# Performance work log

Hardware: AMD Instinct MI355X
Metric: run time of the kernel (lower is better)

Reference implementation:

```python
import jax, jax.numpy as jnp
import numpy as np

B, C, H, W = 8, 256, 64, 64
HID = 4 * C          # mlp_ratio = 4
M = C // 8           # KAttention scale = 8
EPS = 1e-6


def setup_inputs() -> dict:
    key = jax.random.key(0)
    ks = jax.random.split(key, 24)
    n = lambda k, s, sc=1.0: jax.random.normal(k, s, dtype=jnp.float32) * sc
    return {
        "x": n(ks[0], (B, C, H, W)),
        "y": n(ks[1], (B, C, H, W)),
        # shared SeparableConvBN(dim, dim, k=3): 1x1 conv -> depthwise 3x3 -> BN(eval, folded to scale/shift)
        "conv_pw_w": n(ks[2], (C, C), 0.05),
        "conv_dw_w": n(ks[3], (C, 1, 3, 3), 0.1),
        "conv_bn_s": 1.0 + n(ks[4], (C,), 0.1),
        "conv_bn_t": n(ks[5], (C,), 0.1),
        # shared BatchNorm2d(dim) `self.norm` (eval mode, folded)
        "norm_s": 1.0 + n(ks[6], (C,), 0.1),
        "norm_t": n(ks[7], (C,), 0.1),
        # KAttention 1x1 convs (no bias) + gamma
        "q_w": n(ks[8], (M, C), 0.05),
        "k_w": n(ks[9], (M, C), 0.05),
        "v_w": n(ks[10], (C, C), 0.05),
        "gamma_k": n(ks[11], (1,), 0.1),
        # CAttention gamma
        "gamma_c": n(ks[12], (1,), 0.1),
        # Mlp: ConvBN(1x1, bias) -> ReLU6 -> ConvBN(1x1, bias); dropout = identity (eval)
        "fc1_w": n(ks[13], (HID, C), 0.05),
        "fc1_b": n(ks[14], (HID,), 0.05),
        "bn1_s": 1.0 + n(ks[15], (HID,), 0.1),
        "bn1_t": n(ks[16], (HID,), 0.1),
        "fc2_w": n(ks[17], (C, HID), 0.05),
        "fc2_b": n(ks[18], (C,), 0.05),
        "bn2_s": 1.0 + n(ks[19], (C,), 0.1),
        "bn2_t": n(ks[20], (C,), 0.1),
    }


def _bn(x, s, t):
    return x * s[None, :, None, None] + t[None, :, None, None]


def _c1(x, w, b=None):
    # 1x1 conv as channel matmul: [B,C,H,W] x [O,C] -> [B,O,H,W]
    out = jnp.einsum('bchw,oc->bohw', x, w)
    return out if b is None else out + b[None, :, None, None]


def _dw3(x, w):
    # depthwise 3x3, padding=1
    return jax.lax.conv_general_dilated(
        x, w, window_strides=(1, 1), padding='SAME',
        feature_group_count=x.shape[1],
        dimension_numbers=('NCHW', 'OIHW', 'NCHW'))


def reference(x, y, conv_pw_w, conv_dw_w, conv_bn_s, conv_bn_t, norm_s, norm_t,
              q_w, k_w, v_w, gamma_k, gamma_c,
              fc1_w, fc1_b, bn1_s, bn1_t, fc2_w, fc2_b, bn2_s, bn2_t):

    def sepconvbn(z):
        return _bn(_dw3(_c1(z, conv_pw_w), conv_dw_w), conv_bn_s, conv_bn_t)

    def norm(z):
        return _bn(z, norm_s, norm_t)

    def katt(z):
        b, c, h, w = z.shape
        N = h * w
        Q = jax.nn.softplus(_c1(z, q_w)).reshape(b, M, N).transpose(0, 2, 1)  # [b,N,m]
        K = jax.nn.softplus(_c1(z, k_w)).reshape(b, M, N)                    # [b,m,N]
        V = _c1(z, v_w).reshape(b, c, N)                                     # [b,c,N]
        KV = jnp.einsum('bmn,bcn->bmc', K, V)                                # [b,m,c]
        inv = 1.0 / jnp.einsum('bnm,bm->bn', Q, K.sum(-1) + EPS)            # [b,N]
        wv = jnp.einsum('bnm,bmc,bn->bcn', Q, KV, inv)                       # [b,c,N]
        return z + gamma_k[0] * wv.reshape(b, c, h, w)

    def catt(z):
        b, c, h, w = z.shape
        f = z.reshape(b, c, h * w)
        energy = jnp.einsum('bcn,bdn->bcd', f, f)                            # [b,c,c]
        att = jax.nn.softmax(energy.max(-1, keepdims=True) - energy, axis=-1)
        out = jnp.einsum('bcd,bdn->bcn', att, f).reshape(b, c, h, w)
        return gamma_c[0] * out + z

    def light(z):
        return katt(z) + catt(z)

    def mlp(z):
        hdn = jnp.clip(_bn(_c1(z, fc1_w, fc1_b), bn1_s, bn1_t), 0.0, 6.0)  # ReLU6
        return _bn(_c1(hdn, fc2_w, fc2_b), bn2_s, bn2_t)

    x1 = norm(sepconvbn(x))
    ax1 = light(x1)
    y1 = norm(sepconvbn(y))
    ay1 = light(y1)
    x2 = mlp(norm(x1 * ay1))
    y2 = mlp(norm(y1 * ax1))
    y3 = y + y2
    x3 = x + x2 + y3
    return (x3, y3)
```

## Files before the change

### kernel.cpp

```cpp
#include <hip/hip_runtime.h>
#include <hip/hip_bf16.h>
#include <math.h>

typedef __hip_bfloat16 bf16;
typedef unsigned short u16;
#define DEV __device__ __forceinline__

DEV float tofl(float v){ return v; }
DEV float tofl(bf16 v){ return __bfloat162float(v); }
DEV bf16  f2b(float v){ return __float2bfloat16(v); }
DEV u16   f2bu(float v){ bf16 h = f2b(v); u16 u; __builtin_memcpy(&u,&h,2); return u; }
DEV float u2f(u16 u){ bf16 h; __builtin_memcpy(&h,&u,2); return __bfloat162float(h); }

static constexpr int Cc=256, Nn=4096, Mm=32;
static constexpr size_t ACT = (size_t)8*Cc*Nn;
static constexpr float EPSc = 1e-6f;

typedef __attribute__((ext_vector_type(8))) __bf16 bf16x8;
typedef __attribute__((ext_vector_type(4))) float  f32x4;

struct StageRegs { int4 a[4], b[4]; };

DEV void stage_load(const u16* __restrict__ gA, int ldA,
                    const u16* __restrict__ gB, int ldB, int tid, StageRegs& r)
{
  int row = tid>>3, g = tid&7;
#pragma unroll
  for(int i=0;i<4;i++){
    r.a[i] = *(const int4*)(gA + (size_t)(row+32*i)*ldA + g*8);
    r.b[i] = *(const int4*)(gB + (size_t)(row+32*i)*ldB + g*8);
  }
}
DEV void stage_write(u16* __restrict__ sA, u16* __restrict__ sB,
                     int tid, const StageRegs& r)
{
  int row = tid>>3, g = tid&7;
#pragma unroll
  for(int i=0;i<4;i++){
    int rr = row+32*i;
    int gg = ((g ^ (rr&7))<<3);
    *(int4*)(sA + rr*64 + gg) = r.a[i];
    *(int4*)(sB + rr*64 + gg) = r.b[i];
  }
}

template<int KDIM, int OMODE>
__global__ __launch_bounds__(256,2) void gemm_bf16(
    const u16* __restrict__ A, long sAb,
    const u16* __restrict__ B,
    float* __restrict__ Cf, u16* __restrict__ Cb,
    const float* __restrict__ bia, const float* __restrict__ scl,
    const float* __restrict__ sht)
{
  __shared__ __align__(16) u16 sA[2][8192];
  __shared__ __align__(16) u16 sB[2][8192];
  int tid = threadIdx.x;
  int nt = blockIdx.x, mt = blockIdx.y, b = blockIdx.z;
  const u16* gA = A + (size_t)b*sAb + (size_t)mt*128*KDIM;
  const u16* gB = B + ((size_t)b*4096 + (size_t)nt*128)*KDIM;
  int w = tid>>6, l = tid&63;
  int wr = w>>1, wc = w&1;
  int l15 = l&15, lg = l>>4;
  f32x4 acc[4][4] = {};
  StageRegs r;
  stage_load(gA, KDIM, gB, KDIM, tid, r);
  stage_write(sA[0], sB[0], tid, r);
  __syncthreads();
  constexpr int NT = KDIM/64;
  for(int t=0;t<NT;t++){
    int cur = t&1;
    if(t+1<NT) stage_load(gA + (t+1)*64, KDIM, gB + (t+1)*64, KDIM, tid, r);
#pragma unroll
    for(int ks=0;ks<2;ks++){
      bf16x8 af[4], bfr[4];
#pragma unroll
      for(int m=0;m<4;m++){
        int row = wr*64 + m*16 + l15;
        int g = ks*4 + lg;
        af[m] = *(const bf16x8*)(&sA[cur][row*64 + ((g^(row&7))<<3)]);
      }
#pragma unroll
      for(int nn=0;nn<4;nn++){
        int row = wc*64 + nn*16 + l15;
        int g = ks*4 + lg;
        bfr[nn] = *(const bf16x8*)(&sB[cur][row*64 + ((g^(row&7))<<3)]);
      }
#pragma unroll
      for(int m=0;m<4;m++)
#pragma unroll
        for(int nn=0;nn<4;nn++)
          acc[m][nn] = __builtin_amdgcn_mfma_f32_16x16x32_bf16(af[m], bfr[nn], acc[m][nn], 0,0,0);
    }
    if(t+1<NT) stage_write(sA[cur^1], sB[cur^1], tid, r);
    __syncthreads();
  }
  int obase = mt*128 + wr*64;
  int nbase = nt*128 + wc*64;
  if (OMODE==0){
    size_t Mrows = (size_t)gridDim.y*128;
#pragma unroll
    for(int m=0;m<4;m++)
#pragma unroll
      for(int nn=0;nn<4;nn++){
        int o_ = obase + m*16 + (lg<<2);
        int n_ = nbase + nn*16 + l15;
        float* dst = Cf + (((size_t)b*Mrows + o_)<<12) + n_;
#pragma unroll
        for(int i=0;i<4;i++) dst[(size_t)i<<12] = acc[m][nn][i];
      }
  } else {
#pragma unroll
    for(int m=0;m<4;m++)
#pragma unroll
      for(int nn=0;nn<4;nn++){
        int o_ = obase + m*16 + (lg<<2);
        int n_ = nbase + nn*16 + l15;
        union { u16 u[4]; uint2 v; } pk;
#pragma unroll
        for(int i=0;i<4;i++){
          int o = o_+i;
          float a2 = (acc[m][nn][i] + bia[o])*scl[o] + sht[o];
          pk.u[i] = f2bu(fminf(fmaxf(a2,0.f),6.f));
        }
        *(uint2*)(Cb + ((size_t)b*4096 + (size_t)n_)*1024 + o_) = pk.v;
      }
  }
}

template<int KTILES, int KSPLIT, int OMODE>
__global__ __launch_bounds__(256,2) void gemm3(
    const u16* __restrict__ Ah, const u16* __restrict__ Al, int ldA, long sAb,
    const u16* __restrict__ Bh, const u16* __restrict__ Bl, int ldB, long sBb,
    float* __restrict__ Cf)
{
  __shared__ __align__(16) u16 sA[2][8192];
  __shared__ __align__(16) u16 sB[2][8192];
  int tid = threadIdx.x;
  int nt = blockIdx.x, mt = blockIdx.y;
  int b  = blockIdx.z / KSPLIT, ks = blockIdx.z % KSPLIT;
  long koff = (long)ks * (KTILES*64);
  const u16* A0 = Ah + (size_t)b*sAb + (size_t)mt*128*ldA + koff;
  const u16* A1 = Al + (size_t)b*sAb + (size_t)mt*128*ldA + koff;
  const u16* B0 = Bh + (size_t)b*sBb + (size_t)nt*128*ldB + koff;
  const u16* B1 = Bl + (size_t)b*sBb + (size_t)nt*128*ldB + koff;
  int w = tid>>6, l = tid&63;
  int wr = w>>1, wc = w&1;
  int l15 = l&15, lg = l>>4;
  f32x4 acc[4][4] = {};
  StageRegs r;
  for(int pass=0; pass<3; ++pass){
    const u16* gA = (pass==2) ? A1 : A0;
    const u16* gB = (pass==1) ? B1 : B0;
    stage_load(gA, ldA, gB, ldB, tid, r);
    stage_write(sA[0], sB[0], tid, r);
    __syncthreads();
    for(int t=0;t<KTILES;t++){
      int cur = t&1;
      if(t+1<KTILES) stage_load(gA + (t+1)*64, ldA, gB + (t+1)*64, ldB, tid, r);
#pragma unroll
      for(int kss=0;kss<2;kss++){
        bf16x8 af[4], bfr[4];
#pragma unroll
        for(int m=0;m<4;m++){
          int row = wr*64 + m*16 + l15;
          int g = kss*4 + lg;
          af[m] = *(const bf16x8*)(&sA[cur][row*64 + ((g^(row&7))<<3)]);
        }
#pragma unroll
        for(int nn=0;nn<4;nn++){
          int row = wc*64 + nn*16 + l15;
          int g = kss*4 + lg;
          bfr[nn] = *(const bf16x8*)(&sB[cur][row*64 + ((g^(row&7))<<3)]);
        }
#pragma unroll
        for(int m=0;m<4;m++)
#pragma unroll
          for(int nn=0;nn<4;nn++)
            acc[m][nn] = __builtin_amdgcn_mfma_f32_16x16x32_bf16(af[m], bfr[nn], acc[m][nn], 0,0,0);
      }
      if(t+1<KTILES) stage_write(sA[cur^1], sB[cur^1], tid, r);
      __syncthreads();
    }
  }
  int obase = mt*128 + wr*64;
  int nbase = nt*128 + wc*64;
  if (OMODE==0){
    size_t Mrows = (size_t)gridDim.y*128;
#pragma unroll
    for(int m=0;m<4;m++)
#pragma unroll
      for(int nn=0;nn<4;nn++){
        int o_ = obase + m*16 + (lg<<2);
        int n_ = nbase + nn*16 + l15;
        float* dst = Cf + (((size_t)b*Mrows + o_)<<12) + n_;
#pragma unroll
        for(int i=0;i<4;i++) dst[(size_t)i<<12] = acc[m][nn][i];
      }
  } else {
    int gridB = gridDim.z / KSPLIT;
    float* Cb = Cf + ((size_t)ks*gridB + b)*65536;
#pragma unroll
    for(int m=0;m<4;m++)
#pragma unroll
      for(int nn=0;nn<4;nn++){
        int o_ = obase + m*16 + (lg<<2);
        int n_ = nbase + nn*16 + l15;
#pragma unroll
        for(int i=0;i<4;i++) Cb[(size_t)(o_+i)*256 + n_] = acc[m][nn][i];
      }
  }
}

__global__ __launch_bounds__(256) void cvt_w(const float* __restrict__ s,
    u16* __restrict__ d)
{
  int i = blockIdx.x*256 + threadIdx.x;
  d[i] = f2bu(s[i]);
}
__global__ __launch_bounds__(256) void cvt_wsplit(const float* __restrict__ s,
    u16* __restrict__ dh, u16* __restrict__ dl)
{
  int i = blockIdx.x*256 + threadIdx.x;
  float v = s[i];
  u16 h = f2bu(v);
  dh[i] = h; dl[i] = f2bu(v - u2f(h));
}
__global__ __launch_bounds__(256) void cvt_split_nm(const float* __restrict__ x,
    u16* __restrict__ xh, u16* __restrict__ xl)
{
  int n  = blockIdx.x*256 + threadIdx.x;
  int c0 = blockIdx.y*16;
  int b  = blockIdx.z;
  union { u16 u[16]; uint4 q[2]; } ph, pl;
#pragma unroll
  for (int oo=0;oo<16;oo++){
    float v = x[(((size_t)b*256 + c0 + oo)<<12) + n];
    u16 h = f2bu(v);
    ph.u[oo] = h; pl.u[oo] = f2bu(v - u2f(h));
  }
  size_t o = (((size_t)b*4096 + n)<<8) + c0;
  *(uint4*)(xh+o) = ph.q[0]; *(uint4*)(xh+o+8) = ph.q[1];
  *(uint4*)(xl+o) = pl.q[0]; *(uint4*)(xl+o+8) = pl.q[1];
}
__global__ __launch_bounds__(256) void cvt_transpose(const u16* __restrict__ zc,
    u16* __restrict__ zn)
{
  int n  = blockIdx.x*256 + threadIdx.x;
  int c0 = blockIdx.y*16;
  int b  = blockIdx.z;
  union { u16 u[16]; uint4 q[2]; } pk;
#pragma unroll
  for (int oo=0;oo<16;oo++)
    pk.u[oo] = zc[(((size_t)b*256 + c0 + oo)<<12) + n];
  u16* dst = zn + (((size_t)b*4096 + n)<<8) + c0;
  *(uint4*)dst       = pk.q[0];
  *(uint4*)(dst + 8) = pk.q[1];
}

__global__ __launch_bounds__(256) void dw_norm_split(const float* __restrict__ pw,
    u16* __restrict__ zh, u16* __restrict__ zl, const float* __restrict__ dww,
    const float* __restrict__ cbs, const float* __restrict__ cbt,
    const float* __restrict__ ns, const float* __restrict__ nt)
{
  size_t idx = (size_t)blockIdx.x*256 + threadIdx.x;
  int n = (int)(idx & 4095);
  int c = (int)((idx>>12) & 255);
  int h = n>>6, wq = n&63;
  const float* p = pw + (idx - n);
  float acc = 0.f;
  for(int i=0;i<3;i++){
    int hh = h+i-1; if((unsigned)hh >= 64u) continue;
    for(int j=0;j<3;j++){
      int ww = wq+j-1; if((unsigned)ww >= 64u) continue;
      acc += dww[c*9 + i*3 + j] * p[hh*64 + ww];
    }
  }
  float bn = acc*cbs[c] + cbt[c];
  float v  = bn*ns[c] + nt[c];
  u16 hi = f2bu(v);
  zh[idx] = hi; zl[idx] = f2bu(v - u2f(hi));
}

DEV void mac16hl(const u16* __restrict__ hb, const u16* __restrict__ lb,
                 const float* __restrict__ wb, float* __restrict__ acc)
{
  for (int k=0;k<256;k+=4){
    float a0 = u2f(hb[(size_t)(k+0)<<12]) + u2f(lb[(size_t)(k+0)<<12]);
    float a1 = u2f(hb[(size_t)(k+1)<<12]) + u2f(lb[(size_t)(k+1)<<12]);
    float a2 = u2f(hb[(size_t)(k+2)<<12]) + u2f(lb[(size_t)(k+2)<<12]);
    float a3 = u2f(hb[(size_t)(k+3)<<12]) + u2f(lb[(size_t)(k+3)<<12]);
#pragma unroll
    for (int oo=0;oo<16;oo++){
      const float* wr = wb + (size_t)oo*256 + k;
      acc[oo] = fmaf(a3,wr[3],fmaf(a2,wr[2],fmaf(a1,wr[1],fmaf(a0,wr[0],acc[oo]))));
    }
  }
}

__global__ __launch_bounds__(256) void qk_tile(const u16* __restrict__ zh,
    const u16* __restrict__ zl, const float* __restrict__ qw,
    const float* __restrict__ kw, float* __restrict__ Qf, float* __restrict__ Kf)
{
  int n  = blockIdx.x*256 + threadIdx.x;
  int y  = blockIdx.y;
  int o0 = (y&1)*16;
  int b  = blockIdx.z;
  const float* w   = (y<2) ? qw : kw;
  float*       out = (y<2) ? Qf : Kf;
  const u16* hb = zh + (((size_t)b*256)<<12) + n;
  const u16* lb = zl + (((size_t)b*256)<<12) + n;
  float acc[16] = {};
  mac16hl(hb, lb, w + (size_t)o0*256, acc);
#pragma unroll
  for (int oo=0;oo<16;oo++){
    float a = acc[oo];
    a = fmaxf(a,0.f) + log1pf(expf(-fabsf(a)));
    out[(((size_t)b*32 + o0 + oo)<<12) + n] = a;
  }
}

DEV int swz(int r, int j){ return r*128 + ((j ^ ((r>>2)&7))<<2); }

__global__ __launch_bounds__(256) void syrk32(const float* __restrict__ Kf,
    const float* __restrict__ V, float* __restrict__ Cp)
{
  int dt = blockIdx.x, ks = blockIdx.y, b = blockIdx.z;
  __shared__ __align__(16) float sa[32*128];
  __shared__ __align__(16) float sb[32*128];
  int tx = threadIdx.x & 15, ty = threadIdx.x >> 4;
  const float* Ab = Kf + (((size_t)b*32)<<12);
  const float* Bb = V  + (((size_t)b*256 + dt*32)<<12);
  float acc[2][2] = {};
  for (int k0 = ks<<10; k0 < (ks<<10)+1024; k0 += 128){
    __syncthreads();
#pragma unroll
    for (int i=0;i<4;i++){
      int fi = threadIdx.x + i*256;
      int r = fi >> 5, j = fi & 31;
      *(float4*)&sa[swz(r,j)] = *(const float4*)&Ab[((size_t)r<<12) + k0 + (j<<2)];
      *(float4*)&sb[swz(r,j)] = *(const float4*)&Bb[((size_t)r<<12) + k0 + (j<<2)];
    }
    __syncthreads();
#pragma unroll 4
    for (int jj=0;jj<32;jj++){
      float4 av[2], bv[2];
#pragma unroll
      for (int i=0;i<2;i++) av[i] = *(const float4*)&sa[swz(2*ty+i,jj)];
#pragma unroll
      for (int i=0;i<2;i++) bv[i] = *(const float4*)&sb[swz(2*tx+i,jj)];
#pragma unroll
      for (int i=0;i<2;i++)
#pragma unroll
        for (int j2=0;j2<2;j2++)
          acc[i][j2] = fmaf(av[i].w,bv[j2].w, fmaf(av[i].z,bv[j2].z,
                       fmaf(av[i].y,bv[j2].y, fmaf(av[i].x,bv[j2].x, acc[i][j2]))));
    }
  }
  float* Cb = Cp + ((size_t)ks*8 + b)*8192;
#pragma unroll
  for (int i=0;i<2;i++)
#pragma unroll
    for (int j2=0;j2<2;j2++)
      Cb[(size_t)(2*ty+i)*256 + dt*32 + 2*tx + j2] = acc[i][j2];
}

__global__ __launch_bounds__(256) void kv_combine(const float* __restrict__ p,
    float* __restrict__ o)
{
  int i = blockIdx.x*256 + threadIdx.x;
  o[i] = p[i] + p[i+65536] + p[i+131072] + p[i+196608];
}

__global__ __launch_bounds__(256) void softmax16(const float* __restrict__ Ep,
    u16* __restrict__ att)
{
  int bc = blockIdx.x;
  int b = bc>>8, c = bc&255;
  size_t base = (size_t)b*65536 + (size_t)c*256;
  int d = threadIdx.x;
  float ed = 0.f;
#pragma unroll
  for(int ks=0;ks<16;ks++) ed += Ep[base + (size_t)ks*524288 + d];
  __shared__ float red[4];
  int lane = d&63, wid = d>>6;
  float v = ed;
  for (int off=32;off;off>>=1) v = fmaxf(v, __shfl_down(v,off));
  if(lane==0) red[wid]=v;
  __syncthreads();
  float rowmax = fmaxf(fmaxf(red[0],red[1]),fmaxf(red[2],red[3]));
  __syncthreads();
  float s = rowmax - ed;
  float v2 = s;
  for (int off=32;off;off>>=1) v2 = fmaxf(v2, __shfl_down(v2,off));
  if(lane==0) red[wid]=v2;
  __syncthreads();
  float smax = fmaxf(fmaxf(red[0],red[1]),fmaxf(red[2],red[3]));
  __syncthreads();
  float p = expf(s - smax);
  float sv = p;
  for (int off=32;off;off>>=1) sv += __shfl_down(sv,off);
  if(lane==0) red[wid]=sv;
  __syncthreads();
  float sum = red[0]+red[1]+red[2]+red[3];
  att[((size_t)bc<<8)+d] = f2bu(p/sum);
}

__global__ __launch_bounds__(256) void catt_px(const u16* __restrict__ zh,
    const u16* __restrict__ zl, const u16* __restrict__ oh,
    const u16* __restrict__ ol, const float* __restrict__ Qf,
    const float* __restrict__ KVf, const float* __restrict__ invb,
    const float* __restrict__ s1b, const float* __restrict__ gkp,
    const float* __restrict__ gcp, const float* __restrict__ ns,
    const float* __restrict__ nt, u16* __restrict__ px)
{
  int n  = blockIdx.x*256 + threadIdx.x;
  int c0 = blockIdx.y*16;
  int b  = blockIdx.z;
  const float* qb  = Qf  + (((size_t)b*Mm)<<12) + n;
  const float* kvb = KVf + ((size_t)b<<13) + c0;
  float s2[16] = {};
#pragma unroll
  for (int m=0;m<Mm;m++){
    float qm = qb[(size_t)m<<12];
#pragma unroll
    for (int oo=0;oo<16;oo++) s2[oo] = fmaf(qm, kvb[m*256 + oo], s2[oo]);
  }
  float invv = invb[((size_t)b<<12)+n];
  float gk = gkp[0], gc = gcp[0];
  union { u16 u[16]; uint4 q[2]; } pk;
#pragma unroll
  for (int oo=0;oo<16;oo++){
    int c = c0+oo;
    size_t idx = (((size_t)b*256 + c)<<12) + n;
    float zv = u2f(zh[idx]) + u2f(zl[idx]);
    float ov = u2f(oh[idx]) + u2f(ol[idx]);
    float a = 2.f*zv + gc*s1b[idx] + gk*s2[oo]*invv;
    pk.u[oo] = f2bu(ov*a*ns[c] + nt[c]);
  }
  u16* dst = px + (((size_t)b*4096 + n)<<8) + c0;
  *(uint4*)dst       = pk.q[0];
  *(uint4*)(dst + 8) = pk.q[1];
}

__global__ __launch_bounds__(256) void rowsum_lit(const float* __restrict__ A, float* __restrict__ out)
{
  int x = blockIdx.x;
  const float* ar = A + ((size_t)x << 12);
  float a = 0.f;
  for(int n=threadIdx.x; n<Nn; n+=256) a += ar[n];
  __shared__ float red[4];
  for(int off=32;off;off>>=1) a += __shfl_down(a,off);
  int lane = threadIdx.x&63, wid = threadIdx.x>>6;
  if(lane==0) red[wid]=a;
  __syncthreads();
  if(threadIdx.x==0) out[x] = red[0]+red[1]+red[2]+red[3];
}

__global__ __launch_bounds__(256) void inv_lit(const float* __restrict__ Qf,
    const float* __restrict__ Ks, float* __restrict__ invb)
{
  size_t idx = (size_t)blockIdx.x*256 + threadIdx.x;
  int b = (int)(idx>>12);
  const float* qb = Qf + ((size_t)b*Mm << 12) + (int)(idx&4095);
  const float* ks = Ks + b*Mm;
  float s = 0.f;
  for(int m=0;m<Mm;m++) s += qb[(size_t)m<<12]*(ks[m]+EPSc);
  invb[idx] = 1.f/s;
}

__global__ __launch_bounds__(256) void final_y(const float* __restrict__ yin,
    const float* __restrict__ acc, const float* __restrict__ b2,
    const float* __restrict__ s2, const float* __restrict__ t2, float* __restrict__ out)
{
  size_t idx = (size_t)blockIdx.x*256 + threadIdx.x;
  int c = (int)((idx>>12) & 255);
  float y2 = (acc[idx] + b2[c])*s2[c] + t2[c];
  out[ACT + idx] = yin[idx] + y2;
}

__global__ __launch_bounds__(256) void final_x(const float* __restrict__ xin,
    const float* __restrict__ acc, const float* __restrict__ b2,
    const float* __restrict__ s2, const float* __restrict__ t2, float* __restrict__ out)
{
  size_t idx = (size_t)blockIdx.x*256 + threadIdx.x;
  int c = (int)((idx>>12) & 255);
  float x2 = (acc[idx] + b2[c])*s2[c] + t2[c];
  out[idx] = xin[idx] + x2 + out[ACT + idx];
}

extern "C" void kernel_launch(void* const* d_in, const int* in_sizes, int n_in,
                              void* d_out, int out_size, void* d_ws, size_t ws_size,
                              hipStream_t stream)
{
  (void)in_sizes; (void)n_in; (void)out_size; (void)ws_size;
  const float* xin  = (const float*)d_in[0];
  const float* yin  = (const float*)d_in[1];
  const float* pw_w = (const float*)d_in[2];
  const float* dw_w = (const float*)d_in[3];
  const float* cbs  = (const float*)d_in[4];
  const float* cbt  = (const float*)d_in[5];
  const float* ns   = (const float*)d_in[6];
  const float* nt   = (const float*)d_in[7];
  const float* q_w  = (const float*)d_in[8];
  const float* k_w  = (const float*)d_in[9];
  const float* v_w  = (const float*)d_in[10];
  const float* gk   = (const float*)d_in[11];
  const float* gc   = (const float*)d_in[12];
  const float* fc1_w= (const float*)d_in[13];
  const float* fc1_b= (const float*)d_in[14];
  const float* bn1s = (const float*)d_in[15];
  const float* bn1t = (const float*)d_in[16];
  const float* fc2_w= (const float*)d_in[17];
  const float* fc2_b= (const float*)d_in[18];
  const float* bn2s = (const float*)d_in[19];
  const float* bn2t = (const float*)d_in[20];

  char* ws = (char*)d_ws;
  float* A     = (float*)(ws);
  u16*   x1h   = (u16*)  (ws + 33554432);
  u16*   x1l   = (u16*)  (ws + 50331648);
  u16*   y1h   = (u16*)  (ws + 67108864);
  u16*   y1l   = (u16*)  (ws + 83886080);
  u16*   hid   = (u16*)  (ws + 33554432);
  u16*   px_y  = (u16*)  (ws + 100663296);
  u16*   px_x  = (u16*)  (ws + 117440512);
  u16*   xh_nm = (u16*)  (ws + 100663296);
  u16*   xl_nm = (u16*)  (ws + 117440512);
  u16*   z1b   = (u16*)  (ws + 117440512);
  float* Qf    = (float*)(ws + 134217728);
  float* Kf    = (float*)(ws + 138412032);
  u16*   pwh   = (u16*)  (ws + 134217728);
  u16*   pwl   = (u16*)  (ws + 134217728 + 131072);
  u16*   attb  = (u16*)  (ws + 142606336);
  u16*   fc1wb = (u16*)  (ws + 142606336);
  u16*   fc2wb = (u16*)  (ws + 142606336 + 524288);
  float* KVf   = (float*)(ws + 143654912);
  float* Ksf   = (float*)(ws + 143917056);
  float* invb  = (float*)(ws + 143918080);
  float* KVp   = (float*)(ws + 144049152);
  u16*   vwb   = (u16*)  (ws + 144049152);
  float* Ep    = A;
  float* accb  = A;

  dim3 blk(256);
  dim3 gPX(16,16,8), gQK(16,4,8), gKV(8,4,8);
  dim3 gPW(32,2,8), gEn(2,2,128), gG256(32,2,8), gFC1(32,8,8), gFC2(32,2,8);

  cvt_wsplit<<<dim3(256),blk,0,stream>>>(pw_w, pwh, pwl);
  for (int im=0;im<2;im++){
    const float* in = (im==0) ? xin : yin;
    u16* zh = (im==0) ? x1h : y1h;
    u16* zl = (im==0) ? x1l : y1l;
    cvt_split_nm<<<gPX,blk,0,stream>>>(in, xh_nm, xl_nm);
    gemm3<4,1,0><<<gPW,blk,0,stream>>>(pwh, pwl, 256, 0,
                                       xh_nm, xl_nm, 256, 1048576, A);
    dw_norm_split<<<dim3(32768),blk,0,stream>>>(A, zh, zl, dw_w, cbs, cbt, ns, nt);
  }

  for (int t=0;t<2;t++){
    const u16* zh = (t==0) ? x1h : y1h;
    const u16* zl = (t==0) ? x1l : y1l;
    const u16* oh = (t==0) ? y1h : x1h;
    const u16* ol = (t==0) ? y1l : x1l;
    u16* pxout    = (t==0) ? px_y : px_x;
    cvt_w<<<dim3(256),blk,0,stream>>>(v_w, vwb);
    cvt_transpose<<<gPX,blk,0,stream>>>(zh, z1b);
    qk_tile<<<gQK,blk,0,stream>>>(zh, zl, q_w, k_w, Qf, Kf);
    gemm_bf16<256,0><<<gG256,blk,0,stream>>>(vwb, 0, z1b, A, nullptr,
                                             nullptr, nullptr, nullptr);
    syrk32<<<gKV,blk,0,stream>>>(Kf, A, KVp);
    kv_combine<<<dim3(256),blk,0,stream>>>(KVp, KVf);
    rowsum_lit<<<dim3(256),blk,0,stream>>>(Kf, Ksf);
    inv_lit<<<dim3(128),blk,0,stream>>>(Qf, Ksf, invb);
    gemm3<4,16,2><<<gEn,blk,0,stream>>>(zh, zl, 4096, 1048576,
                                        zh, zl, 4096, 1048576, Ep);
    softmax16<<<dim3(2048),blk,0,stream>>>(Ep, attb);
    gemm_bf16<256,0><<<gG256,blk,0,stream>>>(attb, 65536, z1b, A, nullptr,
                                             nullptr, nullptr, nullptr);
    catt_px<<<gPX,blk,0,stream>>>(zh, zl, oh, ol, Qf, KVf, invb, A,
                                  gk, gc, ns, nt, pxout);
  }

  cvt_w<<<dim3(1024),blk,0,stream>>>(fc1_w, fc1wb);
  cvt_w<<<dim3(1024),blk,0,stream>>>(fc2_w, fc2wb);
  for (int s=0;s<2;s++){
    const u16* px = (s==0) ? px_y : px_x;
    gemm_bf16<256,1><<<gFC1,blk,0,stream>>>(fc1wb, 0, px, nullptr, hid,
                                            fc1_b, bn1s, bn1t);
    gemm_bf16<1024,0><<<gFC2,blk,0,stream>>>(fc2wb, 0, hid, accb, nullptr,
                                             nullptr, nullptr, nullptr);
    if (s==0) final_y<<<dim3(32768),blk,0,stream>>>(yin, accb, fc2_b, bn2s, bn2t, (float*)d_out);
    else      final_x<<<dim3(32768),blk,0,stream>>>(xin, accb, fc2_b, bn2s, bn2t, (float*)d_out);
  }
}
```

Before: 865.7 us.

## Move Q/K projection and KV reduction onto bf16 MFMA GEMMs with bf16 intermediates

Replaces the scalar FMA qk_tile and fp32 syrk32 kernels with MFMA-based bf16 GEMMs. Q and K weights are packed into one padded 128-row operand, and K is also written in bf16 so the KV product runs on matrix cores with a 16-way k-split. V and the channel-attention output are now stored as bf16 instead of fp32, halving their write and read traffic. Weight conversion is hoisted out of the loop. The cost is lower precision for Q/K (single bf16 instead of hi/lo split), K, V and the attention output, and half the MFMA work in the padded Q/K and KV GEMMs is discarded.

```diff
diff --git a/kernel.cpp b/kernel.cpp
--- a/kernel.cpp
+++ b/kernel.cpp
@@ -7,7 +7,6 @@
 #define DEV __device__ __forceinline__
 
 DEV float tofl(float v){ return v; }
-DEV float tofl(bf16 v){ return __bfloat162float(v); }
 DEV bf16  f2b(float v){ return __float2bfloat16(v); }
 DEV u16   f2bu(float v){ bf16 h = f2b(v); u16 u; __builtin_memcpy(&u,&h,2); return u; }
 DEV float u2f(u16 u){ bf16 h; __builtin_memcpy(&h,&u,2); return __bfloat162float(h); }
@@ -108,7 +107,7 @@
 #pragma unroll
         for(int i=0;i<4;i++) dst[(size_t)i<<12] = acc[m][nn][i];
       }
-  } else {
+  } else if (OMODE==1){
 #pragma unroll
     for(int m=0;m<4;m++)
 #pragma unroll
@@ -124,7 +123,163 @@
         }
         *(uint2*)(Cb + ((size_t)b*4096 + (size_t)n_)*1024 + o_) = pk.v;
       }
-  }
+  } else {
+    size_t Mrows = (size_t)gridDim.y*128;
+#pragma unroll
+    for(int m=0;m<4;m++)
+#pragma unroll
+      for(int nn=0;nn<4;nn++){
+        int o_ = obase + m*16 + (lg<<2);
+        int n_ = nbase + nn*16 + l15;
+        u16* dst = Cb + (((size_t)b*Mrows + o_)<<12) + n_;
+#pragma unroll
+        for(int i=0;i<4;i++) dst[(size_t)i<<12] = f2bu(acc[m][nn][i]);
+      }
+  }
+}
+
+__global__ __launch_bounds__(256,2) void qk_gemm(
+    const u16* __restrict__ Aqk, const u16* __restrict__ B,
+    float* __restrict__ Qf, float* __restrict__ Kf, u16* __restrict__ Kb)
+{
+  __shared__ __align__(16) u16 sA[2][8192];
+  __shared__ __align__(16) u16 sB[2][8192];
+  int tid = threadIdx.x;
+  int nt = blockIdx.x, b = blockIdx.z;
+  const u16* gA = Aqk;
+  const u16* gB = B + ((size_t)b*4096 + (size_t)nt*128)*256;
+  int w = tid>>6, l = tid&63;
+  int wr = w>>1, wc = w&1;
+  int l15 = l&15, lg = l>>4;
+  f32x4 acc[4][4] = {};
+  StageRegs r;
+  stage_load(gA, 256, gB, 256, tid, r);
+  stage_write(sA[0], sB[0], tid, r);
+  __syncthreads();
+  for(int t=0;t<4;t++){
+    int cur = t&1;
+    if(t+1<4) stage_load(gA + (t+1)*64, 256, gB + (t+1)*64, 256, tid, r);
+#pragma unroll
+    for(int ks=0;ks<2;ks++){
+      bf16x8 af[4], bfr[4];
+#pragma unroll
+      for(int m=0;m<4;m++){
+        int row = wr*64 + m*16 + l15;
+        int g = ks*4 + lg;
+        af[m] = *(const bf16x8*)(&sA[cur][row*64 + ((g^(row&7))<<3)]);
+      }
+#pragma unroll
+      for(int nn=0;nn<4;nn++){
+        int row = wc*64 + nn*16 + l15;
+        int g = ks*4 + lg;
+        bfr[nn] = *(const bf16x8*)(&sB[cur][row*64 + ((g^(row&7))<<3)]);
+      }
+#pragma unroll
+      for(int m=0;m<4;m++)
+#pragma unroll
+        for(int nn=0;nn<4;nn++)
+          acc[m][nn] = __builtin_amdgcn_mfma_f32_16x16x32_bf16(af[m], bfr[nn], acc[m][nn], 0,0,0);
+    }
+    if(t+1<4) stage_write(sA[cur^1], sB[cur^1], tid, r);
+    __syncthreads();
+  }
+  if (wr!=0) return;
+  int nbase = nt*128 + wc*64;
+#pragma unroll
+  for(int m=0;m<4;m++)
+#pragma unroll
+    for(int nn=0;nn<4;nn++){
+      int o_ = m*16 + (lg<<2);
+      int n_ = nbase + nn*16 + l15;
+#pragma unroll
+      for(int i=0;i<4;i++){
+        float a = acc[m][nn][i];
+        a = fmaxf(a,0.f) + log1pf(expf(-fabsf(a)));
+        if (m<2){
+          Qf[(((size_t)b*32 + o_+i)<<12) + n_] = a;
+        } else {
+          int kr = o_+i-32;
+          Kf[(((size_t)b*32 + kr)<<12) + n_] = a;
+          Kb[(((size_t)b*32 + kr)<<12) + n_] = f2bu(a);
+        }
+      }
+    }
+}
+
+__global__ __launch_bounds__(256,2) void kv_gemm(const u16* __restrict__ Kb,
+    const u16* __restrict__ Vb, float* __restrict__ Cp)
+{
+  __shared__ __align__(16) u16 sA[2][8192];
+  __shared__ __align__(16) u16 sB[2][8192];
+  int tid = threadIdx.x;
+  int nt = blockIdx.x;
+  int b  = blockIdx.z >> 4, ks = blockIdx.z & 15;
+  const u16* gA = Kb + ((size_t)b*32)*4096 + ks*256;
+  const u16* gB = Vb + ((size_t)b*256 + (size_t)nt*128)*4096 + ks*256;
+  int row = tid>>3, g = tid&7;
+  int w = tid>>6, l = tid&63;
+  int wr = w>>1, wc = w&1;
+  int l15 = l&15, lg = l>>4;
+  f32x4 acc[4][4] = {};
+  StageRegs r;
+#define KV_LOAD(koff) do { \
+    _Pragma("unroll") \
+    for(int i=0;i<4;i++){ \
+      r.a[i] = *(const int4*)(gA + (size_t)row*4096 + (koff) + g*8); \
+      r.b[i] = *(const int4*)(gB + (size_t)(row+32*i)*4096 + (koff) + g*8); \
+    } } while(0)
+  KV_LOAD(0);
+  stage_write(sA[0], sB[0], tid, r);
+  __syncthreads();
+  for(int t=0;t<4;t++){
+    int cur = t&1;
+    if(t+1<4) KV_LOAD((t+1)*64);
+#pragma unroll
+    for(int kss=0;kss<2;kss++){
+      bf16x8 af[4], bfr[4];
+#pragma unroll
+      for(int m=0;m<4;m++){
+        int rr = wr*64 + m*16 + l15;
+        int gg = kss*4 + lg;
+        af[m] = *(const bf16x8*)(&sA[cur][rr*64 + ((gg^(rr&7))<<3)]);
+      }
+#pragma unroll
+      for(int nn=0;nn<4;nn++){
+        int rr = wc*64 + nn*16 + l15;
+        int gg = kss*4 + lg;
+        bfr[nn] = *(const bf16x8*)(&sB[cur][rr*64 + ((gg^(rr&7))<<3)]);
+      }
+#pragma unroll
+      for(int m=0;m<4;m++)
+#pragma unroll
+        for(int nn=0;nn<4;nn++)
+          acc[m][nn] = __builtin_amdgcn_mfma_f32_16x16x32_bf16(af[m], bfr[nn], acc[m][nn], 0,0,0);
+    }
+    if(t+1<4) stage_write(sA[cur^1], sB[cur^1], tid, r);
+    __syncthreads();
+  }
+#undef KV_LOAD
+  if (wr!=0) return;
+  float* Cb = Cp + ((size_t)ks*8 + b)*8192;
+#pragma unroll
+  for(int m=0;m<2;m++)
+#pragma unroll
+    for(int nn=0;nn<4;nn++){
+      int o_ = m*16 + (lg<<2);
+      int c_ = nt*128 + wc*64 + nn*16 + l15;
+#pragma unroll
+      for(int i=0;i<4;i++) Cb[(size_t)(o_+i)*256 + c_] = acc[m][nn][i];
+    }
+}
+
+__global__ __launch_bounds__(256) void kv_combine16(const float* __restrict__ p,
+    float* __restrict__ o)
+{
+  int i = blockIdx.x*256 + threadIdx.x;
+  float s = 0.f;
+#pragma unroll
+  for(int ks=0;ks<16;ks++) s += p[(size_t)ks*65536 + i];
+  o[i] = s;
 }
 
 template<int KTILES, int KSPLIT, int OMODE>
@@ -225,6 +380,15 @@
   u16 h = f2bu(v);
   dh[i] = h; dl[i] = f2bu(v - u2f(h));
 }
+__global__ __launch_bounds__(256) void cvt_qk(const float* __restrict__ q,
+    const float* __restrict__ k, u16* __restrict__ A)
+{
+  int r = blockIdx.x, c = threadIdx.x;
+  float v = 0.f;
+  if (r < 32) v = q[r*256 + c];
+  else if (r < 64) v = k[(r-32)*256 + c];
+  A[r*256 + c] = f2bu(v);
+}
 __global__ __launch_bounds__(256) void cvt_split_nm(const float* __restrict__ x,
     u16* __restrict__ xh, u16* __restrict__ xl)
 {
@@ -281,96 +445,6 @@
   zh[idx] = hi; zl[idx] = f2bu(v - u2f(hi));
 }
 
-DEV void mac16hl(const u16* __restrict__ hb, const u16* __restrict__ lb,
-                 const float* __restrict__ wb, float* __restrict__ acc)
-{
-  for (int k=0;k<256;k+=4){
-    float a0 = u2f(hb[(size_t)(k+0)<<12]) + u2f(lb[(size_t)(k+0)<<12]);
-    float a1 = u2f(hb[(size_t)(k+1)<<12]) + u2f(lb[(size_t)(k+1)<<12]);
-    float a2 = u2f(hb[(size_t)(k+2)<<12]) + u2f(lb[(size_t)(k+2)<<12]);
-    float a3 = u2f(hb[(size_t)(k+3)<<12]) + u2f(lb[(size_t)(k+3)<<12]);
-#pragma unroll
-    for (int oo=0;oo<16;oo++){
-      const float* wr = wb + (size_t)oo*256 + k;
-      acc[oo] = fmaf(a3,wr[3],fmaf(a2,wr[2],fmaf(a1,wr[1],fmaf(a0,wr[0],acc[oo]))));
-    }
-  }
-}
-
-__global__ __launch_bounds__(256) void qk_tile(const u16* __restrict__ zh,
-    const u16* __restrict__ zl, const float* __restrict__ qw,
-    const float* __restrict__ kw, float* __restrict__ Qf, float* __restrict__ Kf)
-{
-  int n  = blockIdx.x*256 + threadIdx.x;
-  int y  = blockIdx.y;
-  int o0 = (y&1)*16;
-  int b  = blockIdx.z;
-  const float* w   = (y<2) ? qw : kw;
-  float*       out = (y<2) ? Qf : Kf;
-  const u16* hb = zh + (((size_t)b*256)<<12) + n;
-  const u16* lb = zl + (((size_t)b*256)<<12) + n;
-  float acc[16] = {};
-  mac16hl(hb, lb, w + (size_t)o0*256, acc);
-#pragma unroll
-  for (int oo=0;oo<16;oo++){
-    float a = acc[oo];
-    a = fmaxf(a,0.f) + log1pf(expf(-fabsf(a)));
-    out[(((size_t)b*32 + o0 + oo)<<12) + n] = a;
-  }
-}
-
-DEV int swz(int r, int j){ return r*128 + ((j ^ ((r>>2)&7))<<2); }
-
-__global__ __launch_bounds__(256) void syrk32(const float* __restrict__ Kf,
-    const float* __restrict__ V, float* __restrict__ Cp)
-{
-  int dt = blockIdx.x, ks = blockIdx.y, b = blockIdx.z;
-  __shared__ __align__(16) float sa[32*128];
-  __shared__ __align__(16) float sb[32*128];
-  int tx = threadIdx.x & 15, ty = threadIdx.x >> 4;
-  const float* Ab = Kf + (((size_t)b*32)<<12);
-  const float* Bb = V  + (((size_t)b*256 + dt*32)<<12);
-  float acc[2][2] = {};
-  for (int k0 = ks<<10; k0 < (ks<<10)+1024; k0 += 128){
-    __syncthreads();
-#pragma unroll
-    for (int i=0;i<4;i++){
-      int fi = threadIdx.x + i*256;
-      int r = fi >> 5, j = fi & 31;
-      *(float4*)&sa[swz(r,j)] = *(const float4*)&Ab[((size_t)r<<12) + k0 + (j<<2)];
-      *(float4*)&sb[swz(r,j)] = *(const float4*)&Bb[((size_t)r<<12) + k0 + (j<<2)];
-    }
-    __syncthreads();
-#pragma unroll 4
-    for (int jj=0;jj<32;jj++){
-      float4 av[2], bv[2];
-#pragma unroll
-      for (int i=0;i<2;i++) av[i] = *(const float4*)&sa[swz(2*ty+i,jj)];
-#pragma unroll
-      for (int i=0;i<2;i++) bv[i] = *(const float4*)&sb[swz(2*tx+i,jj)];
-#pragma unroll
-      for (int i=0;i<2;i++)
-#pragma unroll
-        for (int j2=0;j2<2;j2++)
-          acc[i][j2] = fmaf(av[i].w,bv[j2].w, fmaf(av[i].z,bv[j2].z,
-                       fmaf(av[i].y,bv[j2].y, fmaf(av[i].x,bv[j2].x, acc[i][j2]))));
-    }
-  }
-  float* Cb = Cp + ((size_t)ks*8 + b)*8192;
-#pragma unroll
-  for (int i=0;i<2;i++)
-#pragma unroll
-    for (int j2=0;j2<2;j2++)
-      Cb[(size_t)(2*ty+i)*256 + dt*32 + 2*tx + j2] = acc[i][j2];
-}
-
-__global__ __launch_bounds__(256) void kv_combine(const float* __restrict__ p,
-    float* __restrict__ o)
-{
-  int i = blockIdx.x*256 + threadIdx.x;
-  o[i] = p[i] + p[i+65536] + p[i+131072] + p[i+196608];
-}
-
 __global__ __launch_bounds__(256) void softmax16(const float* __restrict__ Ep,
     u16* __restrict__ att)
 {
@@ -409,7 +483,7 @@
     const u16* __restrict__ zl, const u16* __restrict__ oh,
     const u16* __restrict__ ol, const float* __restrict__ Qf,
     const float* __restrict__ KVf, const float* __restrict__ invb,
-    const float* __restrict__ s1b, const float* __restrict__ gkp,
+    const u16* __restrict__ s1b, const float* __restrict__ gkp,
     const float* __restrict__ gcp, const float* __restrict__ ns,
     const float* __restrict__ nt, u16* __restrict__ px)
 {
@@ -434,7 +508,7 @@
     size_t idx = (((size_t)b*256 + c)<<12) + n;
     float zv = u2f(zh[idx]) + u2f(zl[idx]);
     float ov = u2f(oh[idx]) + u2f(ol[idx]);
-    float a = 2.f*zv + gc*s1b[idx] + gk*s2[oo]*invv;
+    float a = 2.f*zv + gc*u2f(s1b[idx]) + gk*s2[oo]*invv;
     pk.u[oo] = f2bu(ov*a*ns[c] + nt[c]);
   }
   u16* dst = px + (((size_t)b*4096 + n)<<8) + c0;
@@ -516,7 +590,13 @@
   const float* bn2t = (const float*)d_in[20];
 
   char* ws = (char*)d_ws;
-  float* A     = (float*)(ws);
+  u16*   Vb    = (u16*)  (ws);
+  float* KVp   = (float*)(ws + 16777216);
+  u16*   Kb    = (u16*)  (ws + 20971520);
+  float* Ep    = (float*)(ws);
+  u16*   s1b16 = (u16*)  (ws);
+  float* accb  = (float*)(ws);
+  float* Apw   = (float*)(ws);
   u16*   x1h   = (u16*)  (ws + 33554432);
   u16*   x1l   = (u16*)  (ws + 50331648);
   u16*   y1h   = (u16*)  (ws + 67108864);
@@ -537,14 +617,16 @@
   float* KVf   = (float*)(ws + 143654912);
   float* Ksf   = (float*)(ws + 143917056);
   float* invb  = (float*)(ws + 143918080);
-  float* KVp   = (float*)(ws + 144049152);
   u16*   vwb   = (u16*)  (ws + 144049152);
-  float* Ep    = A;
-  float* accb  = A;
+  u16*   Aqk   = (u16*)  (ws + 144049152 + 131072);
 
   dim3 blk(256);
-  dim3 gPX(16,16,8), gQK(16,4,8), gKV(8,4,8);
-  dim3 gPW(32,2,8), gEn(2,2,128), gG256(32,2,8), gFC1(32,8,8), gFC2(32,2,8);
+  dim3 gPX(16,16,8);
+  dim3 gPW(32,2,8), gEn(2,2,128), gG256(32,2,8), gQKg(32,1,8), gKVg(2,1,128);
+  dim3 gFC1(32,8,8), gFC2(32,2,8);
+
+  cvt_w<<<dim3(256),blk,0,stream>>>(v_w, vwb);
+  cvt_qk<<<dim3(128),blk,0,stream>>>(q_w, k_w, Aqk);
 
   cvt_wsplit<<<dim3(256),blk,0,stream>>>(pw_w, pwh, pwl);
   for (int im=0;im<2;im++){
@@ -553,8 +635,8 @@
     u16* zl = (im==0) ? x1l : y1l;
     cvt_split_nm<<<gPX,blk,0,stream>>>(in, xh_nm, xl_nm);
     gemm3<4,1,0><<<gPW,blk,0,stream>>>(pwh, pwl, 256, 0,
-                                       xh_nm, xl_nm, 256, 1048576, A);
-    dw_norm_split<<<dim3(32768),blk,0,stream>>>(A, zh, zl, dw_w, cbs, cbt, ns, nt);
+                                       xh_nm, xl_nm, 256, 1048576, Apw);
+    dw_norm_split<<<dim3(32768),blk,0,stream>>>(Apw, zh, zl, dw_w, cbs, cbt, ns, nt);
   }
 
   for (int t=0;t<2;t++){
@@ -563,21 +645,20 @@
     const u16* oh = (t==0) ? y1h : x1h;
     const u16* ol = (t==0) ? y1l : x1l;
     u16* pxout    = (t==0) ? px_y : px_x;
-    cvt_w<<<dim3(256),blk,0,stream>>>(v_w, vwb);
     cvt_transpose<<<gPX,blk,0,stream>>>(zh, z1b);
-    qk_tile<<<gQK,blk,0,stream>>>(zh, zl, q_w, k_w, Qf, Kf);
-    gemm_bf16<256,0><<<gG256,blk,0,stream>>>(vwb, 0, z1b, A, nullptr,
+    qk_gemm<<<gQKg,blk,0,stream>>>(Aqk, z1b, Qf, Kf, Kb);
+    gemm_bf16<256,3><<<gG256,blk,0,stream>>>(vwb, 0, z1b, nullptr, Vb,
                                              nullptr, nullptr, nullptr);
-    syrk32<<<gKV,blk,0,stream>>>(Kf, A, KVp);
-    kv_combine<<<dim3(256),blk,0,stream>>>(KVp, KVf);
+    kv_gemm<<<gKVg,blk,0,stream>>>(Kb, Vb, KVp);
+    kv_combine16<<<dim3(256),blk,0,stream>>>(KVp, KVf);
     rowsum_lit<<<dim3(256),blk,0,stream>>>(Kf, Ksf);
     inv_lit<<<dim3(128),blk,0,stream>>>(Qf, Ksf, invb);
     gemm3<4,16,2><<<gEn,blk,0,stream>>>(zh, zl, 4096, 1048576,
                                         zh, zl, 4096, 1048576, Ep);
     softmax16<<<dim3(2048),blk,0,stream>>>(Ep, attb);
-    gemm_bf16<256,0><<<gG256,blk,0,stream>>>(attb, 65536, z1b, A, nullptr,
+    gemm_bf16<256,3><<<gG256,blk,0,stream>>>(attb, 65536, z1b, nullptr, s1b16,
                                              nullptr, nullptr, nullptr);
-    catt_px<<<gPX,blk,0,stream>>>(zh, zl, oh, ol, Qf, KVf, invb, A,
+    catt_px<<<gPX,blk,0,stream>>>(zh, zl, oh, ol, Qf, KVf, invb, s1b16,
                                   gk, gc, ns, nt, pxout);
   }
 
```

New measurement: 769.0 us. 11.2% less time.
